# Performance work log

Measured on AMD Instinct MI355X. Metric: run time of the kernel, lower is better.

## Reference

```python
import jax, jax.numpy as jnp
import numpy as np


def setup_inputs() -> dict:
    key = jax.random.key(0)
    ks = jax.random.split(key, 7)
    B = 65536
    x = jax.random.normal(ks[0], (B, 1, 28, 28), dtype=jnp.float32)
    conv_w = jax.random.normal(ks[1], (4, 1, 7, 7), dtype=jnp.float32) * 0.1
    conv_b = jax.random.normal(ks[2], (4,), dtype=jnp.float32) * 0.1
    fc1_w = jax.random.normal(ks[3], (64, 256), dtype=jnp.float32) * 0.05
    fc1_b = jax.random.normal(ks[4], (64,), dtype=jnp.float32) * 0.05
    fc2_w = jax.random.normal(ks[5], (10, 64), dtype=jnp.float32) * 0.1
    fc2_b = jax.random.normal(ks[6], (10,), dtype=jnp.float32) * 0.1
    return {"x": x, "conv_w": conv_w, "conv_b": conv_b,
            "fc1_w": fc1_w, "fc1_b": fc1_b, "fc2_w": fc2_w, "fc2_b": fc2_b}


def reference(x, conv_w, conv_b, fc1_w, fc1_b, fc2_w, fc2_b):
    # conv1: 1->4 channels, 7x7 kernel, stride 3, no padding -> [B,4,8,8]
    h = jax.lax.conv_general_dilated(
        x, conv_w, window_strides=(3, 3), padding="VALID",
        dimension_numbers=("NCHW", "OIHW", "NCHW"))
    h = h + conv_b[None, :, None, None]
    h = h * h  # SquareFunction (CKKS polynomial activation)
    h = h.reshape(h.shape[0], -1)  # [B, 256]
    h = jnp.einsum("bi,oi->bo", h, fc1_w) + fc1_b
    h = h * h  # SquareFunction
    out = jnp.einsum("bi,oi->bo", h, fc2_w) + fc2_b  # [B, 10]
    return out
```

## Files before the change

kernel.cpp:

```cpp
#include <hip/hip_runtime.h>


#define BLK_IMGS    64
#define CHUNK_IMGS  8
#define NCHUNK      8
#define XCH_FLOATS  (CHUNK_IMGS * 784)

#define LDS_XBUF    0
#define LDS_H       12544
#define LDS_H2      28928
#define LDS_W2      33024
#define LDS_OUT     34048
#define LDS_TOTAL_F 34688

__global__ __launch_bounds__(512, 2)
void encconv_fused2(const float* __restrict__ x,
                    const float* __restrict__ conv_w,
                    const float* __restrict__ conv_b,
                    const float* __restrict__ fc1_w,
                    const float* __restrict__ fc1_b,
                    const float* __restrict__ fc2_w,
                    const float* __restrict__ fc2_b,
                    float* __restrict__ out)
{
    extern __shared__ float lds[];
    float*  xbuf = lds + LDS_XBUF;
    float4* hb   = (float4*)(lds + LDS_H);
    float4* h2b  = (float4*)(lds + LDS_H2);
    float4* w2b  = (float4*)(lds + LDS_W2);
    float*  ob   = lds + LDS_OUT;

    const int tid = threadIdx.x;
    const int blk = blockIdx.x;
    const long base_img = (long)blk * BLK_IMGS;

    const int g  = tid >> 6;
    const int y  = (tid >> 3) & 7;
    const int c  = (tid >> 1) & 3;
    const int xh = tid & 1;

    float wv[49];
    #pragma unroll
    for (int i = 0; i < 49; ++i) wv[i] = conv_w[c * 49 + i];
    const float cb = conv_b[c];

    if (tid < 160) {
        float4 v = *(const float4*)(fc2_w + tid * 4);
        int e  = tid * 4;
        int j  = e >> 6;
        int kk = (e & 63) >> 2;
        w2b[kk * 16 + j] = v;
    }

    const float* xblk = x + base_img * 784;

    float4 pf0, pf1, pf2, pf3;
    {
        const float* src = xblk;
        pf0 = *(const float4*)(src + 4 * tid);
        pf1 = *(const float4*)(src + 4 * (tid + 512));
        pf2 = *(const float4*)(src + 4 * (tid + 1024));
        if (tid < 32) pf3 = *(const float4*)(src + 4 * (tid + 1536));
    }

    for (int ch = 0; ch < NCHUNK; ++ch) {
        float* xb = xbuf + (ch & 1) * XCH_FLOATS;

        *(float4*)(xb + 4 * tid)          = pf0;
        *(float4*)(xb + 4 * (tid + 512))  = pf1;
        *(float4*)(xb + 4 * (tid + 1024)) = pf2;
        if (tid < 32) *(float4*)(xb + 4 * (tid + 1536)) = pf3;
        __syncthreads();

        if (ch + 1 < NCHUNK) {
            const float* src = xblk + (ch + 1) * XCH_FLOATS;
            pf0 = *(const float4*)(src + 4 * tid);
            pf1 = *(const float4*)(src + 4 * (tid + 512));
            pf2 = *(const float4*)(src + 4 * (tid + 1024));
            if (tid < 32) pf3 = *(const float4*)(src + 4 * (tid + 1536));
        }

        float acc0 = 0.f, acc1 = 0.f, acc2 = 0.f, acc3 = 0.f;
        const float* xi = xb + g * 784;
        #pragma unroll
        for (int rr = 0; rr < 7; ++rr) {
            const float* rp = xi + (3 * y + rr) * 28 + 12 * xh;
            float4 r0 = *(const float4*)(rp + 0);
            float4 r1 = *(const float4*)(rp + 4);
            float4 r2 = *(const float4*)(rp + 8);
            float4 r3 = *(const float4*)(rp + 12);
            float r[16] = { r0.x, r0.y, r0.z, r0.w,
                            r1.x, r1.y, r1.z, r1.w,
                            r2.x, r2.y, r2.z, r2.w,
                            r3.x, r3.y, r3.z, r3.w };
            #pragma unroll
            for (int kx = 0; kx < 7; ++kx) {
                const float w = wv[rr * 7 + kx];
                acc0 = fmaf(r[0 + kx], w, acc0);
                acc1 = fmaf(r[3 + kx], w, acc1);
                acc2 = fmaf(r[6 + kx], w, acc2);
                acc3 = fmaf(r[9 + kx], w, acc3);
            }
        }

        float4 hv;
        hv.x = acc0 + cb; hv.x *= hv.x;
        hv.y = acc1 + cb; hv.y *= hv.y;
        hv.z = acc2 + cb; hv.z *= hv.z;
        hv.w = acc3 + cb; hv.w *= hv.w;
        hb[(c * 16 + y * 2 + xh) * 64 + (ch * CHUNK_IMGS + g)] = hv;
    }
    __syncthreads();

    {
        const int img = tid & 63;
        const int w8  = __builtin_amdgcn_readfirstlane(tid >> 6);
        const float* wbase = fc1_w + (w8 * 8) * 256;

        float a0=0.f,a1=0.f,a2=0.f,a3=0.f,a4=0.f,a5=0.f,a6=0.f,a7=0.f;

        #pragma unroll 2
        for (int k4 = 0; k4 < 64; ++k4) {
            float4 h4 = hb[k4 * 64 + img];
            const float* wp = wbase + k4 * 4;
            float4 w0 = *(const float4*)(wp + 0 * 256);
            float4 w1 = *(const float4*)(wp + 1 * 256);
            float4 w2 = *(const float4*)(wp + 2 * 256);
            float4 w3 = *(const float4*)(wp + 3 * 256);
            float4 w4 = *(const float4*)(wp + 4 * 256);
            float4 w5 = *(const float4*)(wp + 5 * 256);
            float4 w6 = *(const float4*)(wp + 6 * 256);
            float4 w7 = *(const float4*)(wp + 7 * 256);
            a0 = fmaf(h4.x,w0.x,a0); a0 = fmaf(h4.y,w0.y,a0); a0 = fmaf(h4.z,w0.z,a0); a0 = fmaf(h4.w,w0.w,a0);
            a1 = fmaf(h4.x,w1.x,a1); a1 = fmaf(h4.y,w1.y,a1); a1 = fmaf(h4.z,w1.z,a1); a1 = fmaf(h4.w,w1.w,a1);
            a2 = fmaf(h4.x,w2.x,a2); a2 = fmaf(h4.y,w2.y,a2); a2 = fmaf(h4.z,w2.z,a2); a2 = fmaf(h4.w,w2.w,a2);
            a3 = fmaf(h4.x,w3.x,a3); a3 = fmaf(h4.y,w3.y,a3); a3 = fmaf(h4.z,w3.z,a3); a3 = fmaf(h4.w,w3.w,a3);
            a4 = fmaf(h4.x,w4.x,a4); a4 = fmaf(h4.y,w4.y,a4); a4 = fmaf(h4.z,w4.z,a4); a4 = fmaf(h4.w,w4.w,a4);
            a5 = fmaf(h4.x,w5.x,a5); a5 = fmaf(h4.y,w5.y,a5); a5 = fmaf(h4.z,w5.z,a5); a5 = fmaf(h4.w,w5.w,a5);
            a6 = fmaf(h4.x,w6.x,a6); a6 = fmaf(h4.y,w6.y,a6); a6 = fmaf(h4.z,w6.z,a6); a6 = fmaf(h4.w,w6.w,a6);
            a7 = fmaf(h4.x,w7.x,a7); a7 = fmaf(h4.y,w7.y,a7); a7 = fmaf(h4.z,w7.z,a7); a7 = fmaf(h4.w,w7.w,a7);
        }

        const float* bp = fc1_b + w8 * 8;
        float4 p0, p1;
        p0.x = a0 + bp[0]; p0.x *= p0.x;
        p0.y = a1 + bp[1]; p0.y *= p0.y;
        p0.z = a2 + bp[2]; p0.z *= p0.z;
        p0.w = a3 + bp[3]; p0.w *= p0.w;
        p1.x = a4 + bp[4]; p1.x *= p1.x;
        p1.y = a5 + bp[5]; p1.y *= p1.y;
        p1.z = a6 + bp[6]; p1.z *= p1.z;
        p1.w = a7 + bp[7]; p1.w *= p1.w;
        h2b[(w8 * 2 + 0) * 64 + img] = p0;
        h2b[(w8 * 2 + 1) * 64 + img] = p1;
    }
    __syncthreads();

    {
        const int im3 = tid >> 3;
        const int q   = tid & 7;

        float s1 = 0.f;
        #pragma unroll
        for (int k4 = 0; k4 < 16; ++k4) {
            float4 hh = h2b[k4 * 64 + im3];
            float4 wA = w2b[k4 * 16 + q];
            s1 = fmaf(hh.x, wA.x, s1); s1 = fmaf(hh.y, wA.y, s1);
            s1 = fmaf(hh.z, wA.z, s1); s1 = fmaf(hh.w, wA.w, s1);
        }
        ob[im3 * 10 + q] = s1 + fc2_b[q];

        if (q < 2) {
            float s2 = 0.f;
            #pragma unroll
            for (int k4 = 0; k4 < 16; ++k4) {
                float4 hh = h2b[k4 * 64 + im3];
                float4 wB = w2b[k4 * 16 + 8 + q];
                s2 = fmaf(hh.x, wB.x, s2); s2 = fmaf(hh.y, wB.y, s2);
                s2 = fmaf(hh.z, wB.z, s2); s2 = fmaf(hh.w, wB.w, s2);
            }
            ob[im3 * 10 + 8 + q] = s2 + fc2_b[8 + q];
        }
    }
    __syncthreads();

    if (tid < 160) {
        float4 v = *(const float4*)(ob + tid * 4);
        *(float4*)(out + (long)blk * 640 + tid * 4) = v;
    }
}

extern "C" void kernel_launch(void* const* d_in, const int* in_sizes, int n_in,
                              void* d_out, int out_size, void* d_ws, size_t ws_size,
                              hipStream_t stream) {
    const float* x      = (const float*)d_in[0];
    const float* conv_w = (const float*)d_in[1];
    const float* conv_b = (const float*)d_in[2];
    const float* fc1_w  = (const float*)d_in[3];
    const float* fc1_b  = (const float*)d_in[4];
    const float* fc2_w  = (const float*)d_in[5];
    const float* fc2_b  = (const float*)d_in[6];
    float* out = (float*)d_out;

    const int B = in_sizes[0] / 784;
    const int blocks = (B + BLK_IMGS - 1) / BLK_IMGS;
    const size_t lds_bytes = LDS_TOTAL_F * sizeof(float);

    static bool attr_set = false;
    if (!attr_set) {
        (void)hipFuncSetAttribute((const void*)encconv_fused2,
                                  hipFuncAttributeMaxDynamicSharedMemorySize,
                                  (int)lds_bytes);
        attr_set = true;
    }

    encconv_fused2<<<blocks, 512, lds_bytes, stream>>>(
        x, conv_w, conv_b, fc1_w, fc1_b, fc2_w, fc2_b, out);
}
```

Before: 357.1 us.

## Use 1024-thread blocks with 16-image chunks and padded conv-output layout

Doubles the block size to 1024 threads so each conv chunk handles 16 images in 4 chunks instead of 8 images in 8 chunks. The x staging buffer becomes single-buffered, with a barrier at the end of each chunk before it is overwritten. The conv-output buffer gets a row pitch of 65 to reduce LDS bank conflicts. The fc1 stage now spreads its 64 outputs over 16 waves, 4 per wave, and the fc2 stage uses only the first 512 threads. This trades the double buffer and adds more barriers and more LDS reads of the activations. The launch-bounds hint of 4 blocks of 1024 threads may also squeeze registers for the 49 conv weights held per thread.

```diff
diff --git a/kernel.cpp b/kernel.cpp
--- a/kernel.cpp
+++ b/kernel.cpp
@@ -2,19 +2,20 @@
 
 
 #define BLK_IMGS    64
-#define CHUNK_IMGS  8
-#define NCHUNK      8
+#define CHUNK_IMGS  16
+#define NCHUNK      4
 #define XCH_FLOATS  (CHUNK_IMGS * 784)
+#define HB_PITCH    65
 
 #define LDS_XBUF    0
 #define LDS_H       12544
-#define LDS_H2      28928
-#define LDS_W2      33024
-#define LDS_OUT     34048
-#define LDS_TOTAL_F 34688
-
-__global__ __launch_bounds__(512, 2)
-void encconv_fused2(const float* __restrict__ x,
+#define LDS_H2      29184
+#define LDS_W2      33280
+#define LDS_OUT     34304
+#define LDS_TOTAL_F 34944
+
+__global__ __launch_bounds__(1024, 4)
+void encconv_fused3(const float* __restrict__ x,
                     const float* __restrict__ conv_w,
                     const float* __restrict__ conv_b,
                     const float* __restrict__ fc1_w,
@@ -58,30 +59,28 @@
     {
         const float* src = xblk;
         pf0 = *(const float4*)(src + 4 * tid);
-        pf1 = *(const float4*)(src + 4 * (tid + 512));
-        pf2 = *(const float4*)(src + 4 * (tid + 1024));
-        if (tid < 32) pf3 = *(const float4*)(src + 4 * (tid + 1536));
+        pf1 = *(const float4*)(src + 4 * (tid + 1024));
+        pf2 = *(const float4*)(src + 4 * (tid + 2048));
+        if (tid < 64) pf3 = *(const float4*)(src + 4 * (tid + 3072));
     }
 
     for (int ch = 0; ch < NCHUNK; ++ch) {
-        float* xb = xbuf + (ch & 1) * XCH_FLOATS;
-
-        *(float4*)(xb + 4 * tid)          = pf0;
-        *(float4*)(xb + 4 * (tid + 512))  = pf1;
-        *(float4*)(xb + 4 * (tid + 1024)) = pf2;
-        if (tid < 32) *(float4*)(xb + 4 * (tid + 1536)) = pf3;
+        *(float4*)(xbuf + 4 * tid)          = pf0;
+        *(float4*)(xbuf + 4 * (tid + 1024)) = pf1;
+        *(float4*)(xbuf + 4 * (tid + 2048)) = pf2;
+        if (tid < 64) *(float4*)(xbuf + 4 * (tid + 3072)) = pf3;
         __syncthreads();
 
         if (ch + 1 < NCHUNK) {
             const float* src = xblk + (ch + 1) * XCH_FLOATS;
             pf0 = *(const float4*)(src + 4 * tid);
-            pf1 = *(const float4*)(src + 4 * (tid + 512));
-            pf2 = *(const float4*)(src + 4 * (tid + 1024));
-            if (tid < 32) pf3 = *(const float4*)(src + 4 * (tid + 1536));
+            pf1 = *(const float4*)(src + 4 * (tid + 1024));
+            pf2 = *(const float4*)(src + 4 * (tid + 2048));
+            if (tid < 64) pf3 = *(const float4*)(src + 4 * (tid + 3072));
         }
 
         float acc0 = 0.f, acc1 = 0.f, acc2 = 0.f, acc3 = 0.f;
-        const float* xi = xb + g * 784;
+        const float* xi = xbuf + g * 784;
         #pragma unroll
         for (int rr = 0; rr < 7; ++rr) {
             const float* rp = xi + (3 * y + rr) * 28 + 12 * xh;
@@ -108,55 +107,43 @@
         hv.y = acc1 + cb; hv.y *= hv.y;
         hv.z = acc2 + cb; hv.z *= hv.z;
         hv.w = acc3 + cb; hv.w *= hv.w;
-        hb[(c * 16 + y * 2 + xh) * 64 + (ch * CHUNK_IMGS + g)] = hv;
-    }
-    __syncthreads();
+        hb[(c * 16 + y * 2 + xh) * HB_PITCH + (ch * CHUNK_IMGS + g)] = hv;
+
+        __syncthreads();
+    }
 
     {
         const int img = tid & 63;
-        const int w8  = __builtin_amdgcn_readfirstlane(tid >> 6);
-        const float* wbase = fc1_w + (w8 * 8) * 256;
-
-        float a0=0.f,a1=0.f,a2=0.f,a3=0.f,a4=0.f,a5=0.f,a6=0.f,a7=0.f;
-
-        #pragma unroll 2
+        const int w4  = __builtin_amdgcn_readfirstlane(tid >> 6);
+        const float* wbase = fc1_w + (w4 * 4) * 256;
+
+        float a0 = 0.f, a1 = 0.f, a2 = 0.f, a3 = 0.f;
+
+        #pragma unroll 4
         for (int k4 = 0; k4 < 64; ++k4) {
-            float4 h4 = hb[k4 * 64 + img];
+            float4 h4 = hb[k4 * HB_PITCH + img];
             const float* wp = wbase + k4 * 4;
             float4 w0 = *(const float4*)(wp + 0 * 256);
             float4 w1 = *(const float4*)(wp + 1 * 256);
             float4 w2 = *(const float4*)(wp + 2 * 256);
             float4 w3 = *(const float4*)(wp + 3 * 256);
-            float4 w4 = *(const float4*)(wp + 4 * 256);
-            float4 w5 = *(const float4*)(wp + 5 * 256);
-            float4 w6 = *(const float4*)(wp + 6 * 256);
-            float4 w7 = *(const float4*)(wp + 7 * 256);
             a0 = fmaf(h4.x,w0.x,a0); a0 = fmaf(h4.y,w0.y,a0); a0 = fmaf(h4.z,w0.z,a0); a0 = fmaf(h4.w,w0.w,a0);
             a1 = fmaf(h4.x,w1.x,a1); a1 = fmaf(h4.y,w1.y,a1); a1 = fmaf(h4.z,w1.z,a1); a1 = fmaf(h4.w,w1.w,a1);
             a2 = fmaf(h4.x,w2.x,a2); a2 = fmaf(h4.y,w2.y,a2); a2 = fmaf(h4.z,w2.z,a2); a2 = fmaf(h4.w,w2.w,a2);
             a3 = fmaf(h4.x,w3.x,a3); a3 = fmaf(h4.y,w3.y,a3); a3 = fmaf(h4.z,w3.z,a3); a3 = fmaf(h4.w,w3.w,a3);
-            a4 = fmaf(h4.x,w4.x,a4); a4 = fmaf(h4.y,w4.y,a4); a4 = fmaf(h4.z,w4.z,a4); a4 = fmaf(h4.w,w4.w,a4);
-            a5 = fmaf(h4.x,w5.x,a5); a5 = fmaf(h4.y,w5.y,a5); a5 = fmaf(h4.z,w5.z,a5); a5 = fmaf(h4.w,w5.w,a5);
-            a6 = fmaf(h4.x,w6.x,a6); a6 = fmaf(h4.y,w6.y,a6); a6 = fmaf(h4.z,w6.z,a6); a6 = fmaf(h4.w,w6.w,a6);
-            a7 = fmaf(h4.x,w7.x,a7); a7 = fmaf(h4.y,w7.y,a7); a7 = fmaf(h4.z,w7.z,a7); a7 = fmaf(h4.w,w7.w,a7);
-        }
-
-        const float* bp = fc1_b + w8 * 8;
-        float4 p0, p1;
+        }
+
+        const float* bp = fc1_b + w4 * 4;
+        float4 p0;
         p0.x = a0 + bp[0]; p0.x *= p0.x;
         p0.y = a1 + bp[1]; p0.y *= p0.y;
         p0.z = a2 + bp[2]; p0.z *= p0.z;
         p0.w = a3 + bp[3]; p0.w *= p0.w;
-        p1.x = a4 + bp[4]; p1.x *= p1.x;
-        p1.y = a5 + bp[5]; p1.y *= p1.y;
-        p1.z = a6 + bp[6]; p1.z *= p1.z;
-        p1.w = a7 + bp[7]; p1.w *= p1.w;
-        h2b[(w8 * 2 + 0) * 64 + img] = p0;
-        h2b[(w8 * 2 + 1) * 64 + img] = p1;
+        h2b[w4 * 64 + img] = p0;
     }
     __syncthreads();
 
-    {
+    if (tid < 512) {
         const int im3 = tid >> 3;
         const int q   = tid & 7;
 
@@ -208,12 +195,12 @@
 
     static bool attr_set = false;
     if (!attr_set) {
-        (void)hipFuncSetAttribute((const void*)encconv_fused2,
+        (void)hipFuncSetAttribute((const void*)encconv_fused3,
                                   hipFuncAttributeMaxDynamicSharedMemorySize,
                                   (int)lds_bytes);
         attr_set = true;
     }
 
-    encconv_fused2<<<blocks, 512, lds_bytes, stream>>>(
+    encconv_fused3<<<blocks, 1024, lds_bytes, stream>>>(
         x, conv_w, conv_b, fc1_w, fc1_b, fc2_w, fc2_b, out);
 }
```

New measurement: 412.6 us. 15.6% more time.
